# Kernel optimization log

Measured on AMD Instinct MI355X. Metric: run time of the kernel, lower is better.

The kernel has to match this reference:

```python
import jax, jax.numpy as jnp
import numpy as np

B, S, E, H, FF = 4, 2048, 1024, 16, 4096
TD = 32  # transition_dim


def _layer_norm(v, g, b, eps=1e-5):
    m = v.mean(-1, keepdims=True)
    var = ((v - m) ** 2).mean(-1, keepdims=True)
    return (v - m) * jax.lax.rsqrt(var + eps) * g + b


def setup_inputs() -> dict:
    key = jax.random.key(0)
    ks = jax.random.split(key, 8)
    w = 0.02
    return {
        "x": jax.random.normal(ks[0], (B, S, E), dtype=jnp.float32),
        "transition_dim": TD,
        "ln1_g": jnp.ones((E,), jnp.float32),
        "ln1_b": jnp.zeros((E,), jnp.float32),
        "ln2_g": jnp.ones((E,), jnp.float32),
        "ln2_b": jnp.zeros((E,), jnp.float32),
        "w_qkv": jax.random.normal(ks[1], (3 * E, E), jnp.float32) * w,
        "b_qkv": jnp.zeros((3 * E,), jnp.float32),
        "w_o": jax.random.normal(ks[2], (E, E), jnp.float32) * w,
        "b_o": jnp.zeros((E,), jnp.float32),
        "w_fc1": jax.random.normal(ks[3], (FF, E), jnp.float32) * w,
        "b_fc1": jnp.zeros((FF,), jnp.float32),
        "w_fc2": jax.random.normal(ks[4], (E, FF), jnp.float32) * w,
        "b_fc2": jnp.zeros((E,), jnp.float32),
    }


def reference(x, transition_dim, ln1_g, ln1_b, ln2_g, ln2_b, w_qkv, b_qkv,
              w_o, b_o, w_fc1, b_fc1, w_fc2, b_fc2):
    Bx, Sx, Ex = x.shape
    Dh = Ex // H
    xn = _layer_norm(x, ln1_g, ln1_b)
    qkv = xn @ w_qkv.T + b_qkv                      # [B,S,3E]
    q, k, v = jnp.split(qkv, 3, axis=-1)
    def heads(t):
        return t.reshape(Bx, Sx, H, Dh).transpose(0, 2, 1, 3)  # [B,H,S,Dh]
    q, k, v = heads(q), heads(k), heads(v)
    scores = jnp.einsum("bhqd,bhkd->bhqk", q, k) / np.sqrt(Dh).astype(np.float32)
    # custom mask: causal (j > i) OR periodic value-column (j % TD == TD-1) blocked
    i = jnp.arange(Sx)
    mask = (i[None, :] > i[:, None]) | ((i[None, :] % transition_dim) == transition_dim - 1)
    scores = jnp.where(mask[None, None], -jnp.inf, scores)
    p = jax.nn.softmax(scores, axis=-1)
    attn = jnp.einsum("bhqk,bhkd->bhqd", p, v)
    attn = attn.transpose(0, 2, 1, 3).reshape(Bx, Sx, Ex)
    attn = attn @ w_o.T + b_o
    x = x + attn
    h = _layer_norm(x, ln2_g, ln2_b)
    h = jax.nn.gelu(h @ w_fc1.T + b_fc1, approximate=False) @ w_fc2.T + b_fc2
    return x + h
```

## Files before the change

kernel.cpp:

```cpp
#include <hip/hip_runtime.h>
#include <hip/hip_bf16.h>

typedef unsigned short u16;
typedef unsigned int u32;
typedef short bf16x8 __attribute__((ext_vector_type(8)));
typedef float f32x4 __attribute__((ext_vector_type(4)));
typedef float f32x16 __attribute__((ext_vector_type(16)));

#define B_ 4
#define S_ 2048
#define E_ 1024
#define H_ 16
#define FF_ 4096
#define M_ 8192

__device__ __forceinline__ u16 f2bf(float f) {
    u32 u = __float_as_uint(f);
    u32 r = (u + 0x7FFFu + ((u >> 16) & 1u)) >> 16;
    return (u16)r;
}
__device__ __forceinline__ float bf2f(u16 v) {
    return __uint_as_float(((u32)v) << 16);
}
__device__ __forceinline__ u32 cvtpk(float lo, float hi) {
    u32 r;
    asm("v_cvt_pk_bf16_f32 %0, %1, %2" : "=v"(r) : "v"(lo), "v"(hi));
    return r;
}
__device__ __forceinline__ void pswap(u32& a, u32& b) {
    asm("v_permlane32_swap_b32 %0, %1" : "+v"(a), "+v"(b));
}
__device__ __forceinline__ void gload16(const void* g, void* l) {
    __builtin_amdgcn_global_load_lds(
        (__attribute__((address_space(1))) void*)g,
        (__attribute__((address_space(3))) void*)l, 16, 0, 0);
}
__device__ __forceinline__ float gelu_f(float v) {
    float y = 0.79788456f * (v + 0.044715f * v * v * v);
    float t = __builtin_amdgcn_exp2f(2.88539008f * y);
    float th = 1.0f - 2.0f / (t + 1.0f);
    return 0.5f * v * (1.0f + th);
}

__global__ __launch_bounds__(256) void cvt4_kernel(const float* __restrict__ s0, u16* __restrict__ d0,
                                                   const float* __restrict__ s1, u16* __restrict__ d1,
                                                   const float* __restrict__ s2, u16* __restrict__ d2,
                                                   const float* __restrict__ s3, u16* __restrict__ d3) {
    int blk = blockIdx.x;
    const float* s; u16* d; int base;
    if (blk < 3072)      { s = s0; d = d0; base = blk; }
    else if (blk < 4096) { s = s1; d = d1; base = blk - 3072; }
    else if (blk < 8192) { s = s2; d = d2; base = blk - 4096; }
    else                 { s = s3; d = d3; base = blk - 8192; }
    int i = base * 256 + threadIdx.x;
    float4 v = ((const float4*)s)[i];
    ushort4 o;
    o.x = f2bf(v.x); o.y = f2bf(v.y); o.z = f2bf(v.z); o.w = f2bf(v.w);
    ((ushort4*)d)[i] = o;
}

__global__ __launch_bounds__(256) void vtrans_kernel(const u16* __restrict__ qkv,
                                                     u16* __restrict__ vt) {
    __shared__ u16 tile[64 * 67];
    int t = threadIdx.x;
    int st = blockIdx.x;
    int bh = blockIdx.y;
    int b = bh >> 4, h = bh & 15;
    int s0 = st * 64;
    int r = t >> 3, c0 = (t & 7) * 8;
#pragma unroll
    for (int half = 0; half < 2; half++) {
        int rr = r + half * 32;
        const u16* src = qkv + (size_t)(b * S_ + s0 + rr) * 3072 + 2048 + h * 64 + c0;
        uint4 v = *(const uint4*)src;
        u16* pv = (u16*)&v;
#pragma unroll
        for (int e = 0; e < 8; e++) tile[(c0 + e) * 67 + rr] = pv[e];
    }
    __syncthreads();
    int d = t >> 2, ch = t & 3;
    u16 buf[16];
#pragma unroll
    for (int j = 0; j < 16; j++) buf[j] = tile[d * 67 + ch * 16 + j];
    u16* dst = vt + ((size_t)bh * 64 + d) * 2048 + s0 + ch * 16;
    *(uint4*)dst = *(uint4*)&buf[0];
    *(uint4*)(dst + 8) = *(uint4*)&buf[8];
}

__global__ __launch_bounds__(256) void ln_kernel(const float* __restrict__ x,
                                                 const float* __restrict__ g,
                                                 const float* __restrict__ bb,
                                                 u16* __restrict__ out) {
    int row = blockIdx.x;
    int t = threadIdx.x;
    const float4* xr = (const float4*)(x + (size_t)row * E_);
    float4 v = xr[t];
    float s = v.x + v.y + v.z + v.w;
    float sq = v.x * v.x + v.y * v.y + v.z * v.z + v.w * v.w;
    for (int o = 1; o < 64; o <<= 1) {
        s += __shfl_xor(s, o, 64);
        sq += __shfl_xor(sq, o, 64);
    }
    __shared__ float ss[4], sqs[4];
    int w = t >> 6, l = t & 63;
    if (l == 0) { ss[w] = s; sqs[w] = sq; }
    __syncthreads();
    s = ss[0] + ss[1] + ss[2] + ss[3];
    sq = sqs[0] + sqs[1] + sqs[2] + sqs[3];
    float mean = s * (1.0f / E_);
    float var = sq * (1.0f / E_) - mean * mean;
    float rstd = rsqrtf(var + 1e-5f);
    float4 gv = ((const float4*)g)[t];
    float4 bv = ((const float4*)bb)[t];
    ushort4 o4;
    o4.x = f2bf((v.x - mean) * rstd * gv.x + bv.x);
    o4.y = f2bf((v.y - mean) * rstd * gv.y + bv.y);
    o4.z = f2bf((v.z - mean) * rstd * gv.z + bv.z);
    o4.w = f2bf((v.w - mean) * rstd * gv.w + bv.w);
    ((ushort4*)(out + (size_t)row * E_))[t] = o4;
}

template <int EPI>
__global__ __launch_bounds__(512, 2) void gemm256m(const u16* __restrict__ A,
                                                   const u16* __restrict__ Bt,
                                                   const float* __restrict__ bias,
                                                   void* __restrict__ outp,
                                                   int N, int K) {
    __shared__ u16 ldsA[2 * 2 * 8192];
    __shared__ u16 ldsB[2 * 2 * 8192];
    int t = threadIdx.x;
    int wid = t >> 6, l = t & 63, l15 = l & 15, hi4 = l >> 4;
    int wm = wid >> 2, wn = wid & 3;

    int nwg = gridDim.x;
    int flat = blockIdx.x;
    int swz = (flat & 7) * (nwg >> 3) + (flat >> 3);
    int nx = N >> 8;
    int nxs = nx >> 2;
    int sid = swz >> 4, wi = swz & 15;
    int sidm = sid / nxs, sidn = sid % nxs;
    int m0 = (sidm * 4 + (wi >> 2)) * 256;
    int n0 = (sidn * 4 + (wi & 3)) * 256;
    const size_t Kb = (size_t)K * 2;

    f32x4 acc[8][4];
    f32x4 zf = {0.f, 0.f, 0.f, 0.f};
#pragma unroll
    for (int i = 0; i < 8; i++)
#pragma unroll
        for (int j = 0; j < 4; j++) acc[i][j] = zf;

    auto stageA = [&](int buf, int h, int k0) {
#pragma unroll
        for (int rr = 0; rr < 2; ++rr) {
            int o = t * 16 + rr * 8192;
            int lr = o >> 7;
            int gch = ((o >> 4) & 7) ^ (lr & 7);
            int grow = m0 + (lr >> 6) * 128 + h * 64 + (lr & 63);
            gload16((const char*)A + (size_t)grow * Kb + k0 * 2 + gch * 16,
                    (char*)ldsA + (buf * 2 + h) * 16384 + o);
        }
    };
    auto stageB = [&](int buf, int h, int k0) {
#pragma unroll
        for (int rr = 0; rr < 2; ++rr) {
            int o = t * 16 + rr * 8192;
            int lr = o >> 7;
            int gch = ((o >> 4) & 7) ^ (lr & 7);
            int grow = n0 + (lr >> 5) * 64 + h * 32 + (lr & 31);
            gload16((const char*)Bt + (size_t)grow * Kb + k0 * 2 + gch * 16,
                    (char*)ldsB + (buf * 2 + h) * 16384 + o);
        }
    };

    auto readA = [&](int bq, int mh, bf16x8 (&af)[4][2]) {
#pragma unroll
        for (int mi = 0; mi < 4; mi++)
#pragma unroll
            for (int ks = 0; ks < 2; ks++) {
                int lr = wm * 64 + mi * 16 + l15;
                int ob = lr * 128 + ks * 64 + hi4 * 16;
                af[mi][ks] = *(const bf16x8*)((const char*)ldsA +
                             (bq * 2 + mh) * 16384 + (ob ^ ((lr & 7) << 4)));
            }
    };
    auto readB = [&](int bq, int nh, bf16x8 (&bfr)[2][2]) {
#pragma unroll
        for (int nq = 0; nq < 2; nq++)
#pragma unroll
            for (int ks = 0; ks < 2; ks++) {
                int lr = wn * 32 + nq * 16 + l15;
                int ob = lr * 128 + ks * 64 + hi4 * 16;
                bfr[nq][ks] = *(const bf16x8*)((const char*)ldsB +
                              (bq * 2 + nh) * 16384 + (ob ^ ((lr & 7) << 4)));
            }
    };
    auto mma = [&](bf16x8 (&af)[4][2], bf16x8 (&bfr)[2][2], int mh, int nh) {
#pragma unroll
        for (int mi = 0; mi < 4; mi++)
#pragma unroll
            for (int nq = 0; nq < 2; nq++)
#pragma unroll
                for (int ks = 0; ks < 2; ks++)
                    acc[mh * 4 + mi][nh * 2 + nq] =
                        __builtin_amdgcn_mfma_f32_16x16x32_bf16(
                            af[mi][ks], bfr[nq][ks], acc[mh * 4 + mi][nh * 2 + nq], 0, 0, 0);
    };

#define GWAIT(N)                                            \
    asm volatile("s_waitcnt vmcnt(" #N ")" ::: "memory");   \
    __builtin_amdgcn_sched_barrier(0);
#define PH_MID                                              \
    __builtin_amdgcn_s_barrier();                           \
    asm volatile("s_waitcnt lgkmcnt(0)" ::: "memory");      \
    __builtin_amdgcn_sched_barrier(0);                      \
    __builtin_amdgcn_s_setprio(1);
#define PH_END                                              \
    __builtin_amdgcn_s_setprio(0);                          \
    __builtin_amdgcn_s_barrier();

    int ITERS = K >> 7;
    stageB(0, 0, 0); stageB(0, 1, 0); stageA(0, 0, 0); stageA(0, 1, 0);
    stageB(1, 0, 64); stageB(1, 1, 64); stageA(1, 0, 64);
    GWAIT(6);
    __builtin_amdgcn_s_barrier();
    for (int s = 0; s < ITERS; ++s) {
        int k1 = (2 * s + 1) << 6;
        int k2 = (2 * s + 2) << 6; if (k2 >= K) k2 = 0;
        int k3 = (2 * s + 3) << 6; if (k3 >= K) k3 = 0;
        bf16x8 af[4][2], b0[2][2], b1[2][2];
        readA(0, 0, af); readB(0, 0, b0); readB(0, 1, b1);
        stageA(1, 1, k1);
        PH_MID; mma(af, b0, 0, 0); mma(af, b1, 0, 1); PH_END;
        readA(0, 1, af);
        stageB(0, 0, k2); stageB(0, 1, k2); stageA(0, 0, k2);
        PH_MID; mma(af, b0, 1, 0); mma(af, b1, 1, 1);
        __builtin_amdgcn_s_setprio(0);
        GWAIT(8);
        __builtin_amdgcn_s_barrier();
        readA(1, 0, af); readB(1, 0, b0); readB(1, 1, b1);
        stageA(0, 1, k2);
        PH_MID; mma(af, b0, 0, 0); mma(af, b1, 0, 1);
        __builtin_amdgcn_s_setprio(0);
        GWAIT(8);
        __builtin_amdgcn_s_barrier();
        readA(1, 1, af);
        stageB(1, 0, k3); stageB(1, 1, k3); stageA(1, 0, k3);
        GWAIT(6);
        PH_MID; mma(af, b0, 1, 0); mma(af, b1, 1, 1); PH_END;
    }
    GWAIT(0);
    __builtin_amdgcn_s_barrier();
#undef GWAIT
#undef PH_MID
#undef PH_END

    float bias_v[4];
#pragma unroll
    for (int nf = 0; nf < 4; nf++) bias_v[nf] = bias[n0 + wn * 64 + nf * 16 + l15];

    u16* myl = (wid < 4 ? ldsA : ldsB) + (wid & 3) * 8192;
#pragma unroll
    for (int mf = 0; mf < 8; mf++)
#pragma unroll
        for (int nf = 0; nf < 4; nf++)
#pragma unroll
            for (int j = 0; j < 4; j++) {
                int row = mf * 16 + hi4 * 4 + j;
                int col = nf * 16 + l15;
                float v = acc[mf][nf][j] + bias_v[nf];
                if (EPI == 2) v = gelu_f(v);
                int chunk = ((col >> 3) + (row >> 2)) & 7;
                myl[row * 64 + chunk * 8 + (col & 7)] = f2bf(v);
            }
    u16* out16 = (u16*)outp;
#pragma unroll
    for (int pass = 0; pass < 16; ++pass) {
        int row = pass * 8 + (l >> 3);
        int chunk = ((l & 7) + (row >> 2)) & 7;
        uint4 d = *(const uint4*)&myl[row * 64 + chunk * 8];
        int grow = m0 + wm * 128 + row;
        int gcol = n0 + wn * 64 + (l & 7) * 8;
        *(uint4*)&out16[(size_t)grow * N + gcol] = d;
    }
}

template <int EPI>
__global__ __launch_bounds__(512, 2) void gemm256n128(const u16* __restrict__ A,
                                                      const u16* __restrict__ Bt,
                                                      const float* __restrict__ bias,
                                                      void* __restrict__ outp,
                                                      const float* __restrict__ resid,
                                                      int N, int K) {
    __shared__ u16 ldsA[2 * 2 * 8192];
    __shared__ u16 ldsB[2 * 8192];
    int t = threadIdx.x;
    int wid = t >> 6, l = t & 63, l15 = l & 15, hi4 = l >> 4;
    int wm = wid >> 2, wn = wid & 3;

    int nwg = gridDim.x;
    int flat = blockIdx.x;
    int swz = (flat & 7) * (nwg >> 3) + (flat >> 3);
    int nx = N >> 7;
    int nxs = nx >> 2;
    int sid = swz >> 4, wi = swz & 15;
    int sidm = sid / nxs, sidn = sid % nxs;
    int m0 = (sidm * 4 + (wi >> 2)) * 256;
    int n0 = (sidn * 4 + (wi & 3)) * 128;
    const size_t Kb = (size_t)K * 2;

    f32x4 acc[8][2];
    f32x4 zf = {0.f, 0.f, 0.f, 0.f};
#pragma unroll
    for (int i = 0; i < 8; i++)
#pragma unroll
        for (int j = 0; j < 2; j++) acc[i][j] = zf;

    auto stageA = [&](int buf, int h, int k0) {
#pragma unroll
        for (int rr = 0; rr < 2; ++rr) {
            int o = t * 16 + rr * 8192;
            int lr = o >> 7;
            int gch = ((o >> 4) & 7) ^ (lr & 7);
            int grow = m0 + (lr >> 6) * 128 + h * 64 + (lr & 63);
            gload16((const char*)A + (size_t)grow * Kb + k0 * 2 + gch * 16,
                    (char*)ldsA + (buf * 2 + h) * 16384 + o);
        }
    };
    auto stageB = [&](int buf, int k0) {
#pragma unroll
        for (int rr = 0; rr < 2; ++rr) {
            int o = t * 16 + rr * 8192;
            int lr = o >> 7;
            int gch = ((o >> 4) & 7) ^ (lr & 7);
            int grow = n0 + lr;
            gload16((const char*)Bt + (size_t)grow * Kb + k0 * 2 + gch * 16,
                    (char*)ldsB + buf * 16384 + o);
        }
    };

    auto readA = [&](int bq, int mh, bf16x8 (&af)[4][2]) {
#pragma unroll
        for (int mi = 0; mi < 4; mi++)
#pragma unroll
            for (int ks = 0; ks < 2; ks++) {
                int lr = wm * 64 + mi * 16 + l15;
                int ob = lr * 128 + ks * 64 + hi4 * 16;
                af[mi][ks] = *(const bf16x8*)((const char*)ldsA +
                             (bq * 2 + mh) * 16384 + (ob ^ ((lr & 7) << 4)));
            }
    };
    auto readB = [&](int bq, bf16x8 (&bfr)[2][2]) {
#pragma unroll
        for (int nq = 0; nq < 2; nq++)
#pragma unroll
            for (int ks = 0; ks < 2; ks++) {
                int lr = wn * 32 + nq * 16 + l15;
                int ob = lr * 128 + ks * 64 + hi4 * 16;
                bfr[nq][ks] = *(const bf16x8*)((const char*)ldsB +
                              bq * 16384 + (ob ^ ((lr & 7) << 4)));
            }
    };
    auto mma = [&](bf16x8 (&af)[4][2], bf16x8 (&bfr)[2][2], int mh) {
#pragma unroll
        for (int mi = 0; mi < 4; mi++)
#pragma unroll
            for (int nq = 0; nq < 2; nq++)
#pragma unroll
                for (int ks = 0; ks < 2; ks++)
                    acc[mh * 4 + mi][nq] =
                        __builtin_amdgcn_mfma_f32_16x16x32_bf16(
                            af[mi][ks], bfr[nq][ks], acc[mh * 4 + mi][nq], 0, 0, 0);
    };

#define GWAIT(N)                                            \
    asm volatile("s_waitcnt vmcnt(" #N ")" ::: "memory");   \
    __builtin_amdgcn_sched_barrier(0);
#define PH_MID                                              \
    __builtin_amdgcn_s_barrier();                           \
    asm volatile("s_waitcnt lgkmcnt(0)" ::: "memory");      \
    __builtin_amdgcn_sched_barrier(0);                      \
    __builtin_amdgcn_s_setprio(1);
#define PH_END                                              \
    __builtin_amdgcn_s_setprio(0);                          \
    __builtin_amdgcn_s_barrier();

    int ITERS = K >> 7;
    stageB(0, 0); stageA(0, 0, 0); stageA(0, 1, 0);
    stageB(1, 64); stageA(1, 0, 64);
    GWAIT(4);
    __builtin_amdgcn_s_barrier();
    for (int s = 0; s < ITERS; ++s) {
        int k1 = (2 * s + 1) << 6;
        int k2 = (2 * s + 2) << 6; if (k2 >= K) k2 = 0;
        int k3 = (2 * s + 3) << 6; if (k3 >= K) k3 = 0;
        bf16x8 af[4][2], br[2][2];
        readA(0, 0, af); readB(0, br); stageA(1, 1, k1);
        PH_MID; mma(af, br, 0); PH_END;
        readA(0, 1, af); stageB(0, k2); stageA(0, 0, k2); GWAIT(4);
        PH_MID; mma(af, br, 1); PH_END;
        readA(1, 0, af); readB(1, br); stageA(0, 1, k2);
        PH_MID; mma(af, br, 0); PH_END;
        readA(1, 1, af); stageB(1, k3); stageA(1, 0, k3); GWAIT(4);
        PH_MID; mma(af, br, 1); PH_END;
    }
    GWAIT(0);
#undef GWAIT
#undef PH_MID
#undef PH_END

    float bias_v[2];
#pragma unroll
    for (int nq = 0; nq < 2; nq++) bias_v[nq] = bias[n0 + wn * 32 + nq * 16 + l15];

#pragma unroll
    for (int mf = 0; mf < 8; mf++)
#pragma unroll
        for (int nq = 0; nq < 2; nq++)
#pragma unroll
            for (int j = 0; j < 4; j++) {
                int row = m0 + wm * 128 + mf * 16 + hi4 * 4 + j;
                int col = n0 + wn * 32 + nq * 16 + l15;
                float v = acc[mf][nq][j] + bias_v[nq];
                size_t idx = (size_t)row * N + col;
                if (EPI == 1)
                    ((float*)outp)[idx] = resid[idx] + v;
                else
                    ((u16*)outp)[idx] = f2bf(v);
            }
}

__global__ __launch_bounds__(128) void attn_kernel(const u16* __restrict__ qkv,
                                                   const u16* __restrict__ vt,
                                                   u16* __restrict__ aout) {
    __shared__ u16 Ksb[2 * 4096];
    __shared__ u16 Vsb[2 * 4096];
    int t = threadIdx.x;
    int wv = t >> 6, l = t & 63;
    int q31 = l & 31, hi = l >> 5;
    int flat = blockIdx.x;
    int logical = (flat & 7) * 128 + (flat >> 3);
    int bh = logical >> 4, p0 = logical & 15;
    int b = bh >> 4, h = bh & 15;

    const float qs = 0.18033688011f;

    const char* srcK0 = (const char*)(qkv + E_ + (size_t)(b * S_ + (t >> 3)) * 3072 + h * 64) +
                        ((t & 7) ^ ((t >> 3) & 7)) * 16;
    const char* srcV0 = (const char*)(vt + ((size_t)(bh * 64 + (t >> 3))) * 2048) +
                        ((t & 7) ^ ((t >> 3) & 7)) * 16;
    auto issueK = [&](int buf, int j0) {
#pragma unroll
        for (int pp = 0; pp < 4; pp++)
            gload16(srcK0 + (size_t)pp * 98304 + (size_t)j0 * 6144,
                    (char*)Ksb + buf * 8192 + 16 * t + 2048 * pp);
    };
    auto issueV = [&](int buf, int j0) {
#pragma unroll
        for (int pp = 0; pp < 4; pp++)
            gload16(srcV0 + (size_t)pp * 65536 + (size_t)j0 * 2,
                    (char*)Vsb + buf * 8192 + 16 * t + 2048 * pp);
    };

    f32x16 zf16;
#pragma unroll
    for (int r = 0; r < 16; r++) zf16[r] = 0.f;

    for (int half = 0; half < 2; ++half) {
        int qt = half ? (31 - p0) : p0;
        int rowq = qt * 64 + wv * 32 + q31;

        bf16x8 qreg[4];
        const u16* qbase = qkv + (size_t)(b * S_ + rowq) * 3072 + h * 64 + hi * 8;
#pragma unroll
        for (int g = 0; g < 4; g++) qreg[g] = *(const bf16x8*)(qbase + 16 * g);

        f32x16 o0 = zf16, o1 = zf16;
        float lrun = 0.f;

        int j1 = (qt >= 1) ? 64 : 0;
        issueK(0, 0); issueV(0, 0);
        issueK(1, j1); issueV(1, j1);

        for (int jt = 0; jt <= qt; ++jt) {
            int cur = jt & 1;
            int j0 = jt * 64;
            asm volatile("s_waitcnt vmcnt(8)" ::: "memory");
            __builtin_amdgcn_sched_barrier(0);
            __builtin_amdgcn_s_barrier();

            const u16* Kc = Ksb + cur * 4096;
            const u16* Vc = Vsb + cur * 4096;

            f32x16 s0 = zf16, s1 = zf16;
            __builtin_amdgcn_s_setprio(1);
#pragma unroll
            for (int g = 0; g < 4; g++) {
                int r0 = q31, r1 = 32 + q31;
                bf16x8 k0 = *(const bf16x8*)&Kc[((r0 << 6) + hi * 8 + 16 * g) ^ ((r0 & 7) << 3)];
                bf16x8 k1 = *(const bf16x8*)&Kc[((r1 << 6) + hi * 8 + 16 * g) ^ ((r1 & 7) << 3)];
                s0 = __builtin_amdgcn_mfma_f32_32x32x16_bf16(k0, qreg[g], s0, 0, 0, 0);
                s1 = __builtin_amdgcn_mfma_f32_32x32x16_bf16(k1, qreg[g], s1, 0, 0, 0);
            }
            __builtin_amdgcn_s_setprio(0);

            int cb0 = j0 + 4 * hi;
            float sa = 0.f, sb = 0.f, sc2 = 0.f, sd = 0.f;
            if (jt == qt) {
#pragma unroll
                for (int r = 0; r < 16; r++) {
                    const int cc = (r & 3) + 8 * (r >> 2);
                    bool bad0 = (cb0 + cc > rowq) || (r == 15 && hi);
                    bool bad1 = (cb0 + 32 + cc > rowq) || (r == 15 && hi);
                    float p0 = bad0 ? 0.f : __builtin_amdgcn_exp2f(s0[r] * qs);
                    float p1 = bad1 ? 0.f : __builtin_amdgcn_exp2f(s1[r] * qs);
                    s0[r] = p0; s1[r] = p1;
                    if (r & 1) { sb += p0; sd += p1; } else { sa += p0; sc2 += p1; }
                }
            } else {
#pragma unroll
                for (int r = 0; r < 16; r++) {
                    float p0 = __builtin_amdgcn_exp2f(s0[r] * qs);
                    float p1 = __builtin_amdgcn_exp2f(s1[r] * qs);
                    if (r == 15 && hi) { p0 = 0.f; p1 = 0.f; }
                    s0[r] = p0; s1[r] = p1;
                    if (r & 1) { sb += p0; sd += p1; } else { sa += p0; sc2 += p1; }
                }
            }
            lrun += (sa + sb) + (sc2 + sd);

            bf16x8 pa[4];
#pragma unroll
            for (int g = 0; g < 4; g++) {
                const int bs = (g & 1) * 8;
                u32 wa, wb, wc, wd;
                if (g < 2) {
                    wa = cvtpk(s0[bs + 0], s0[bs + 1]);
                    wb = cvtpk(s0[bs + 4], s0[bs + 5]);
                    wc = cvtpk(s0[bs + 2], s0[bs + 3]);
                    wd = cvtpk(s0[bs + 6], s0[bs + 7]);
                } else {
                    wa = cvtpk(s1[bs + 0], s1[bs + 1]);
                    wb = cvtpk(s1[bs + 4], s1[bs + 5]);
                    wc = cvtpk(s1[bs + 2], s1[bs + 3]);
                    wd = cvtpk(s1[bs + 6], s1[bs + 7]);
                }
                pswap(wa, wb);
                pswap(wc, wd);
                union { u32 w[4]; bf16x8 f; } u;
                u.w[0] = wa; u.w[1] = wc; u.w[2] = wb; u.w[3] = wd;
                pa[g] = u.f;
            }

            __builtin_amdgcn_s_setprio(1);
#pragma unroll
            for (int g = 0; g < 4; g++) {
                int d0 = q31, d1 = 32 + q31;
                bf16x8 v0 = *(const bf16x8*)&Vc[((d0 << 6) + hi * 8 + 16 * g) ^ ((d0 & 7) << 3)];
                bf16x8 v1 = *(const bf16x8*)&Vc[((d1 << 6) + hi * 8 + 16 * g) ^ ((d1 & 7) << 3)];
                o0 = __builtin_amdgcn_mfma_f32_32x32x16_bf16(v0, pa[g], o0, 0, 0, 0);
                o1 = __builtin_amdgcn_mfma_f32_32x32x16_bf16(v1, pa[g], o1, 0, 0, 0);
            }
            __builtin_amdgcn_s_setprio(0);

            __builtin_amdgcn_s_barrier();
            int nj = (jt + 2 <= qt) ? (jt + 2) * 64 : 0;
            issueK(cur, nj);
            issueV(cur, nj);
        }

        lrun += __shfl_xor(lrun, 32, 64);
        float inv = 1.0f / lrun;
        u16* orow = aout + (size_t)(b * S_ + rowq) * E_ + h * 64 + 4 * hi;
#pragma unroll
        for (int r = 0; r < 16; r++) {
            const int cc = (r & 3) + 8 * (r >> 2);
            orow[cc] = f2bf(o0[r] * inv);
            orow[32 + cc] = f2bf(o1[r] * inv);
        }

        if (half == 0) {
            asm volatile("s_waitcnt vmcnt(0)" ::: "memory");
            __builtin_amdgcn_sched_barrier(0);
            __builtin_amdgcn_s_barrier();
        }
    }
}

extern "C" void kernel_launch(void* const* d_in, const int* in_sizes, int n_in,
                              void* d_out, int out_size, void* d_ws, size_t ws_size,
                              hipStream_t stream) {
    const float* x = (const float*)d_in[0];
    const float* ln1_g = (const float*)d_in[2];
    const float* ln1_b = (const float*)d_in[3];
    const float* ln2_g = (const float*)d_in[4];
    const float* ln2_b = (const float*)d_in[5];
    const float* w_qkv = (const float*)d_in[6];
    const float* b_qkv = (const float*)d_in[7];
    const float* w_o = (const float*)d_in[8];
    const float* b_o = (const float*)d_in[9];
    const float* w_fc1 = (const float*)d_in[10];
    const float* b_fc1 = (const float*)d_in[11];
    const float* w_fc2 = (const float*)d_in[12];
    const float* b_fc2 = (const float*)d_in[13];
    float* out = (float*)d_out;
    char* ws = (char*)d_ws;

    u16* wqkv_bf = (u16*)(ws);
    u16* wo_bf   = (u16*)(ws + 6291456);
    u16* wfc1_bf = (u16*)(ws + 8388608);
    u16* wfc2_bf = (u16*)(ws + 16777216);
    u16* xn_bf   = (u16*)(ws + 25165824);
    u16* qkv_bf  = (u16*)(ws + 41943040);
    u16* ffn1_bf = (u16*)(ws + 41943040);
    u16* attn_bf = (u16*)(ws + 92274688);
    float* x2    = (float*)(ws + 109051904);
    u16* vtw     = (u16*)(ws + 109051904);
    (void)in_sizes; (void)n_in; (void)out_size; (void)ws_size;

    cvt4_kernel<<<12288, 256, 0, stream>>>(w_qkv, wqkv_bf, w_o, wo_bf,
                                           w_fc1, wfc1_bf, w_fc2, wfc2_bf);

    ln_kernel<<<M_, 256, 0, stream>>>(x, ln1_g, ln1_b, xn_bf);

    gemm256m<0><<<384, 512, 0, stream>>>(xn_bf, wqkv_bf, b_qkv, qkv_bf, 3072, 1024);

    vtrans_kernel<<<dim3(32, 64), 256, 0, stream>>>(qkv_bf, vtw);

    attn_kernel<<<1024, 128, 0, stream>>>(qkv_bf, vtw, attn_bf);

    gemm256n128<1><<<256, 512, 0, stream>>>(attn_bf, wo_bf, b_o, x2, x, 1024, 1024);

    ln_kernel<<<M_, 256, 0, stream>>>(x2, ln2_g, ln2_b, xn_bf);

    gemm256m<2><<<512, 512, 0, stream>>>(xn_bf, wfc1_bf, b_fc1, ffn1_bf, 4096, 1024);

    gemm256n128<1><<<256, 512, 0, stream>>>(ffn1_bf, wfc2_bf, b_fc2, out, x2, 1024, 4096);
}
```

Baseline: 361.7 us.

## Stage bf16 GEMM epilogue through LDS for coalesced stores; use n128 GEMM for QKV

The bf16-output epilogue of the n128 GEMM now writes each wave's tile into a swizzled LDS buffer and then emits 16-byte row-contiguous global stores, replacing scattered 2-byte stores. The QKV projection switches from the 256-wide gemm256m kernel to gemm256n128 with twice as many blocks. This is meant to cut uncoalesced write traffic and improve CU occupancy and load balance for the QKV GEMM. It adds a barrier and reuses the A-tile LDS region after the main loop, and the smaller N tile may lower per-block data reuse.

```diff
diff --git a/kernel.cpp b/kernel.cpp
--- a/kernel.cpp
+++ b/kernel.cpp
@@ -413,21 +413,46 @@
 #pragma unroll
     for (int nq = 0; nq < 2; nq++) bias_v[nq] = bias[n0 + wn * 32 + nq * 16 + l15];
 
-#pragma unroll
-    for (int mf = 0; mf < 8; mf++)
-#pragma unroll
-        for (int nq = 0; nq < 2; nq++)
-#pragma unroll
-            for (int j = 0; j < 4; j++) {
-                int row = m0 + wm * 128 + mf * 16 + hi4 * 4 + j;
-                int col = n0 + wn * 32 + nq * 16 + l15;
-                float v = acc[mf][nq][j] + bias_v[nq];
-                size_t idx = (size_t)row * N + col;
-                if (EPI == 1)
+    if constexpr (EPI == 0) {
+        __builtin_amdgcn_s_barrier();
+        u16* myl = ldsA + wid * 4096;
+#pragma unroll
+        for (int mf = 0; mf < 8; mf++)
+#pragma unroll
+            for (int nq = 0; nq < 2; nq++)
+#pragma unroll
+                for (int j = 0; j < 4; j++) {
+                    int row = mf * 16 + hi4 * 4 + j;
+                    int col = nq * 16 + l15;
+                    float v = acc[mf][nq][j] + bias_v[nq];
+                    int chunk = ((col >> 3) + (row >> 2)) & 3;
+                    myl[row * 32 + chunk * 8 + (col & 7)] = f2bf(v);
+                }
+        u16* out16 = (u16*)outp;
+#pragma unroll
+        for (int pass = 0; pass < 8; ++pass) {
+            int row = pass * 16 + (l >> 2);
+            int cc = l & 3;
+            int chunk = (cc + (row >> 2)) & 3;
+            uint4 d = *(const uint4*)&myl[row * 32 + chunk * 8];
+            int grow = m0 + wm * 128 + row;
+            int gcol = n0 + wn * 32 + cc * 8;
+            *(uint4*)&out16[(size_t)grow * N + gcol] = d;
+        }
+    } else {
+#pragma unroll
+        for (int mf = 0; mf < 8; mf++)
+#pragma unroll
+            for (int nq = 0; nq < 2; nq++)
+#pragma unroll
+                for (int j = 0; j < 4; j++) {
+                    int row = m0 + wm * 128 + mf * 16 + hi4 * 4 + j;
+                    int col = n0 + wn * 32 + nq * 16 + l15;
+                    float v = acc[mf][nq][j] + bias_v[nq];
+                    size_t idx = (size_t)row * N + col;
                     ((float*)outp)[idx] = resid[idx] + v;
-                else
-                    ((u16*)outp)[idx] = f2bf(v);
-            }
+                }
+    }
 }
 
 __global__ __launch_bounds__(128) void attn_kernel(const u16* __restrict__ qkv,
@@ -623,7 +648,7 @@
 
     ln_kernel<<<M_, 256, 0, stream>>>(x, ln1_g, ln1_b, xn_bf);
 
-    gemm256m<0><<<384, 512, 0, stream>>>(xn_bf, wqkv_bf, b_qkv, qkv_bf, 3072, 1024);
+    gemm256n128<0><<<768, 512, 0, stream>>>(xn_bf, wqkv_bf, b_qkv, qkv_bf, nullptr, 3072, 1024);
 
     vtrans_kernel<<<dim3(32, 64), 256, 0, stream>>>(qkv_bf, vtw);
 
```

New measurement: 360.9 us. About the same (-0.2%).
